# Kernel tuning notes

Measured on AMD Instinct MI355X. Metric: run time of the kernel, lower is better.

Reference implementation:

```python
import jax, jax.numpy as jnp
import numpy as np

# --- module constants (from init_kwargs) ---
R_HRS = 1000000.0   # high-resistance state (ohm)
R_LRS = 1000.0      # low-resistance state (ohm)
PARASITIC_R = 2.0   # wire resistance per crossbar segment (ohm)
BITS = 4            # conductance quantization bits
BATCH, IN_F, OUT_F = 8192, 1024, 1024


def weight_mapping(W, R_hrs, R_lrs):
    # linearly map weights into the [G_hrs, G_lrs] conductance window
    G_hrs, G_lrs = 1.0 / R_hrs, 1.0 / R_lrs
    Wmin, Wmax = W.min(), W.max()
    return (W - Wmin) / (Wmax - Wmin) * (G_lrs - G_hrs) + G_hrs


def quantization(G, R_lrs, R_hrs, bits):
    # snap conductances to 2**bits uniform levels in [G_hrs, G_lrs]
    G_hrs, G_lrs = 1.0 / R_hrs, 1.0 / R_lrs
    step = (G_lrs - G_hrs) / (2 ** bits - 1)
    return jnp.round((G - G_hrs) / step) * step + G_hrs


def ideal_model(G, x, parasitic_r):
    # ideal crossbar: I = V @ G  (no IR drop)
    return x @ G


def jeong_model(G, x, parasitic_r):
    # Jeong-style analytical IR-drop model: each cell (i, j) sees an extra
    # series wire resistance r*((j+1) segments along its word line +
    # (rows - i) segments along its bit line).
    rows, cols = G.shape  # [in, out]
    r_series = parasitic_r * (
        (jnp.arange(cols, dtype=G.dtype) + 1.0)[None, :]
        + (rows - jnp.arange(rows, dtype=G.dtype))[:, None]
    )  # [in, out]
    G_eff = 1.0 / (1.0 / G + r_series)
    return x @ G_eff  # [batch, out]


def output_unmapping(Wt, currents, x, R_hrs, R_lrs):
    # invert the affine conductance mapping: G = a*W + b  =>  x@W = (I - b*sum(x))/a
    G_hrs, G_lrs = 1.0 / R_hrs, 1.0 / R_lrs
    Wmin, Wmax = Wt.min(), Wt.max()
    a = (G_lrs - G_hrs) / (Wmax - Wmin)
    b = G_hrs - a * Wmin
    return (currents - b * x.sum(axis=1, keepdims=True)) / a


def setup_inputs() -> dict:
    key = jax.random.key(0)
    k1, k2, k3 = jax.random.split(key, 3)
    x = jax.random.uniform(k1, (BATCH, IN_F), dtype=jnp.float32)          # read voltages in [0,1)
    weight = jax.random.normal(k2, (OUT_F, IN_F), dtype=jnp.float32) * 0.1
    bias = jax.random.normal(k3, (OUT_F,), dtype=jnp.float32) * 0.01
    return {"x": x, "weight": weight, "bias": bias}


def reference(x, weight, bias):
    Wt = weight.T  # [in, out], matches self.weight.T in the torch module
    conductances = quantization(weight_mapping(Wt, R_HRS, R_LRS), R_LRS, R_HRS, BITS)
    currents = jeong_model(conductances, x, PARASITIC_R)          # non-ideal simulation
    ideal_currents = ideal_model(conductances, x, PARASITIC_R)    # bias-correction pass
    correction = currents.mean(axis=1) / ideal_currents.mean(axis=1)  # [batch]
    output = output_unmapping(Wt, currents, x, R_HRS, R_LRS)      # [batch, out]
    return output + bias[None, :] * correction[:, None]
```

## Files before the change

kernel.cpp:

```cpp
#include <hip/hip_runtime.h>
#include <hip/hip_bf16.h>
#include <cstdint>

#define BATCH 8192
#define IN_F  1024
#define OUT_F 1024
#define G_HRS 1e-6f
#define G_LRS 1e-3f
#define PAR_R 2.0f
#define LEVELS 15.0f

#define WS_MM    0
#define WS_VEFF  4096
#define WS_VID   8192
#define WS_CORR  16384
#define WS_BT    65536
#define WS_ABF   (65536 + 2097152)
#define WS_NEED_FULL  (WS_ABF + (size_t)BATCH * IN_F * 2)
#define WS_NEED_MIN   ((size_t)WS_ABF)

__device__ __forceinline__ unsigned short f2bf(float f) {
    union { float f; unsigned int i; } v; v.f = f;
    unsigned int u = v.i;
    unsigned int r = (u + 0x7FFFu + ((u >> 16) & 1u)) >> 16;
    return (unsigned short)r;
}
__device__ __forceinline__ unsigned int fmap(float f) {
    union { float f; unsigned int u; } v; v.f = f;
    return (v.u & 0x80000000u) ? ~v.u : (v.u | 0x80000000u);
}
__device__ __forceinline__ float funmap(unsigned int m) {
    union { unsigned int u; float f; } v;
    v.u = (m & 0x80000000u) ? (m & 0x7FFFFFFFu) : ~m;
    return v.f;
}
__device__ __forceinline__ float quant_g(float wv, float wmin, float inv_range) {
    float t = (wv - wmin) * inv_range;
    float step = (G_LRS - G_HRS) / LEVELS;
    return rintf(t * LEVELS) * step + G_HRS;
}

__global__ void kinit(unsigned int* mm) {
    if (threadIdx.x == 0) { mm[0] = 0u; mm[1] = 0xFFFFFFFFu; }
}

__global__ void kminmax(const float* __restrict__ w, unsigned int* mm) {
    int tid = blockIdx.x * blockDim.x + threadIdx.x;
    int stride = gridDim.x * blockDim.x;
    float lo = 1e30f, hi = -1e30f;
    const float4* w4 = (const float4*)w;
    const int n4 = (IN_F * OUT_F) / 4;
    for (int i = tid; i < n4; i += stride) {
        float4 q = w4[i];
        lo = fminf(lo, fminf(fminf(q.x, q.y), fminf(q.z, q.w)));
        hi = fmaxf(hi, fmaxf(fmaxf(q.x, q.y), fmaxf(q.z, q.w)));
    }
#pragma unroll
    for (int m = 1; m < 64; m <<= 1) {
        lo = fminf(lo, __shfl_xor(lo, m, 64));
        hi = fmaxf(hi, __shfl_xor(hi, m, 64));
    }
    if ((threadIdx.x & 63) == 0) {
        atomicMax(&mm[0], fmap(hi));
        atomicMin(&mm[1], fmap(lo));
    }
}

__global__ void kbuild(const float* __restrict__ w, const unsigned int* __restrict__ mm,
                       unsigned short* __restrict__ bt) {
    float wmax = funmap(mm[0]), wmin = funmap(mm[1]);
    float inv_range = 1.0f / (wmax - wmin);
    float acoef = (G_LRS - G_HRS) * inv_range;
    float bcoef = G_HRS - acoef * wmin;
    float inva = 1.0f / acoef;
    int n = blockIdx.x;
    int k0 = threadIdx.x * 4;
    float4 q = *(const float4*)&w[n * IN_F + k0];
    float wv[4] = { q.x, q.y, q.z, q.w };
    unsigned short o[4];
#pragma unroll
    for (int j = 0; j < 4; j++) {
        int k = k0 + j;
        float g = quant_g(wv[j], wmin, inv_range);
        float r = PAR_R * ((float)(n + 1) + (float)(IN_F - k));
        float ge = 1.0f / (1.0f / g + r);
        o[j] = f2bf((ge - bcoef) * inva);
    }
    uint2 ov;
    ov.x = (unsigned int)o[0] | ((unsigned int)o[1] << 16);
    ov.y = (unsigned int)o[2] | ((unsigned int)o[3] << 16);
    *(uint2*)&bt[n * IN_F + k0] = ov;
}

__global__ void kvec(const float* __restrict__ w, const unsigned int* __restrict__ mm,
                     float* __restrict__ veff, float* __restrict__ vid) {
    float wmax = funmap(mm[0]), wmin = funmap(mm[1]);
    float inv_range = 1.0f / (wmax - wmin);
    int k = blockIdx.x;
    float se = 0.f, si = 0.f;
    for (int n = threadIdx.x; n < OUT_F; n += blockDim.x) {
        float g = quant_g(w[n * IN_F + k], wmin, inv_range);
        float r = PAR_R * ((float)(n + 1) + (float)(IN_F - k));
        se += 1.0f / (1.0f / g + r);
        si += g;
    }
#pragma unroll
    for (int m = 1; m < 64; m <<= 1) {
        se += __shfl_xor(se, m, 64);
        si += __shfl_xor(si, m, 64);
    }
    __shared__ float red[8];
    int wv = threadIdx.x >> 6, ln = threadIdx.x & 63;
    if (ln == 0) { red[wv] = se; red[4 + wv] = si; }
    __syncthreads();
    if (threadIdx.x == 0) {
        veff[k] = red[0] + red[1] + red[2] + red[3];
        vid[k]  = red[4] + red[5] + red[6] + red[7];
    }
}

__global__ void kcorr(const float* __restrict__ x, const float* __restrict__ veff,
                      const float* __restrict__ vid, float* __restrict__ corr,
                      unsigned short* __restrict__ abf) {
    int row = blockIdx.x;
    int k0 = threadIdx.x * 4;
    float4 q = *(const float4*)&x[(size_t)row * IN_F + k0];
    if (abf) {
        uint2 ov;
        ov.x = (unsigned int)f2bf(q.x) | ((unsigned int)f2bf(q.y) << 16);
        ov.y = (unsigned int)f2bf(q.z) | ((unsigned int)f2bf(q.w) << 16);
        *(uint2*)&abf[(size_t)row * IN_F + k0] = ov;
    }
    float se = q.x * veff[k0] + q.y * veff[k0 + 1] + q.z * veff[k0 + 2] + q.w * veff[k0 + 3];
    float si = q.x * vid[k0]  + q.y * vid[k0 + 1]  + q.z * vid[k0 + 2]  + q.w * vid[k0 + 3];
#pragma unroll
    for (int m = 1; m < 64; m <<= 1) {
        se += __shfl_xor(se, m, 64);
        si += __shfl_xor(si, m, 64);
    }
    __shared__ float red[8];
    int wv = threadIdx.x >> 6, ln = threadIdx.x & 63;
    if (ln == 0) { red[wv] = se; red[4 + wv] = si; }
    __syncthreads();
    if (threadIdx.x == 0)
        corr[row] = (red[0] + red[1] + red[2] + red[3]) / (red[4] + red[5] + red[6] + red[7]);
}

typedef __attribute__((ext_vector_type(8))) short bf16x8;
typedef __attribute__((ext_vector_type(4))) float f32x4;

#define GLD_LDS16(g, l) \
    __builtin_amdgcn_global_load_lds((const __attribute__((address_space(1))) void*)(g), \
                                     (__attribute__((address_space(3))) void*)(l), 16, 0, 0)

template <bool CONVA>
__global__ __launch_bounds__(256) void kgemm(
    const float* __restrict__ Af32,
    const unsigned short* __restrict__ Abf,
    const unsigned short* __restrict__ Bt,
    const float* __restrict__ bias,
    const float* __restrict__ corr,
    float* __restrict__ out)
{
    __shared__ unsigned short As[128 * 32];
    __shared__ unsigned short Bs[128 * 32];
    const int tid = threadIdx.x;
    const int bm = blockIdx.x * 128;
    const int bn = blockIdx.y * 128;
    const int wave = tid >> 6, lane = tid & 63;
    const int wmL = (wave >> 1) * 64;
    const int wnL = (wave & 1) * 64;
    const int fr = lane & 15;
    const int fk = (lane >> 4) * 8;
    const int quad = lane >> 4;

    f32x4 acc[4][4] = {};

    const int c0 = tid, c1 = tid + 256;
    const unsigned short* gB0 = Bt + (size_t)(bn + (c0 >> 2)) * IN_F + ((c0 & 3) << 3);
    const unsigned short* gB1 = Bt + (size_t)(bn + (c1 >> 2)) * IN_F + ((c1 & 3) << 3);
    const unsigned short* gA0 = nullptr; const unsigned short* gA1 = nullptr;
    const float* fA0 = nullptr; const float* fA1 = nullptr;
    if (CONVA) {
        fA0 = Af32 + (size_t)(bm + (c0 >> 2)) * IN_F + ((c0 & 3) << 3);
        fA1 = Af32 + (size_t)(bm + (c1 >> 2)) * IN_F + ((c1 & 3) << 3);
    } else {
        gA0 = Abf + (size_t)(bm + (c0 >> 2)) * IN_F + ((c0 & 3) << 3);
        gA1 = Abf + (size_t)(bm + (c1 >> 2)) * IN_F + ((c1 & 3) << 3);
    }

    for (int kb = 0; kb < IN_F; kb += 32) {
        uint2 cv0, cv1;
        if (CONVA) {
            float4 p0 = *(const float4*)(fA0 + kb);
            float4 p1 = *(const float4*)(fA0 + kb + 4);
            float4 p2 = *(const float4*)(fA1 + kb);
            float4 p3 = *(const float4*)(fA1 + kb + 4);
            cv0.x = (unsigned int)f2bf(p0.x) | ((unsigned int)f2bf(p0.y) << 16);
            cv0.y = (unsigned int)f2bf(p0.z) | ((unsigned int)f2bf(p0.w) << 16);
            uint2 cv0b; cv0b.x = (unsigned int)f2bf(p1.x) | ((unsigned int)f2bf(p1.y) << 16);
            cv0b.y = (unsigned int)f2bf(p1.z) | ((unsigned int)f2bf(p1.w) << 16);
            uint2 cv1a; cv1a.x = (unsigned int)f2bf(p2.x) | ((unsigned int)f2bf(p2.y) << 16);
            cv1a.y = (unsigned int)f2bf(p2.z) | ((unsigned int)f2bf(p2.w) << 16);
            uint2 cv1b; cv1b.x = (unsigned int)f2bf(p3.x) | ((unsigned int)f2bf(p3.y) << 16);
            cv1b.y = (unsigned int)f2bf(p3.z) | ((unsigned int)f2bf(p3.w) << 16);
            __syncthreads();
            *(uint4*)&As[c0 * 8] = make_uint4(cv0.x, cv0.y, cv0b.x, cv0b.y);
            *(uint4*)&As[c1 * 8] = make_uint4(cv1a.x, cv1a.y, cv1b.x, cv1b.y);
            GLD_LDS16(gB0 + kb, &Bs[c0 * 8]);
            GLD_LDS16(gB1 + kb, &Bs[c1 * 8]);
        } else {
            __syncthreads();
            GLD_LDS16(gA0 + kb, &As[c0 * 8]);
            GLD_LDS16(gA1 + kb, &As[c1 * 8]);
            GLD_LDS16(gB0 + kb, &Bs[c0 * 8]);
            GLD_LDS16(gB1 + kb, &Bs[c1 * 8]);
        }
        __syncthreads();

        bf16x8 af[4], bfv[4];
#pragma unroll
        for (int mt = 0; mt < 4; mt++)
            af[mt] = *(const bf16x8*)&As[(wmL + mt * 16 + fr) * 32 + fk];
#pragma unroll
        for (int nt = 0; nt < 4; nt++)
            bfv[nt] = *(const bf16x8*)&Bs[(wnL + nt * 16 + fr) * 32 + fk];
#pragma unroll
        for (int mt = 0; mt < 4; mt++)
#pragma unroll
            for (int nt = 0; nt < 4; nt++)
                acc[mt][nt] = __builtin_amdgcn_mfma_f32_16x16x32_bf16(af[mt], bfv[nt], acc[mt][nt], 0, 0, 0);
    }

#pragma unroll
    for (int nt = 0; nt < 4; nt++) {
        int gc = bn + wnL + nt * 16 + fr;
        float bv = bias[gc];
#pragma unroll
        for (int mt = 0; mt < 4; mt++) {
#pragma unroll
            for (int r = 0; r < 4; r++) {
                int gr = bm + wmL + mt * 16 + quad * 4 + r;
                out[(size_t)gr * OUT_F + gc] = acc[mt][nt][r] + bv * corr[gr];
            }
        }
    }
}

extern "C" void kernel_launch(void* const* d_in, const int* in_sizes, int n_in,
                              void* d_out, int out_size, void* d_ws, size_t ws_size,
                              hipStream_t stream) {
    const float* x    = (const float*)d_in[0];
    const float* w    = (const float*)d_in[1];
    const float* bias = (const float*)d_in[2];
    float* out = (float*)d_out;

    char* ws = (char*)d_ws;
    unsigned int* mm   = (unsigned int*)(ws + WS_MM);
    float* veff        = (float*)(ws + WS_VEFF);
    float* vid         = (float*)(ws + WS_VID);
    float* corr        = (float*)(ws + WS_CORR);
    unsigned short* bt = (unsigned short*)(ws + WS_BT);
    unsigned short* abf = (unsigned short*)(ws + WS_ABF);

    bool full = ws_size >= WS_NEED_FULL;

    kinit<<<1, 64, 0, stream>>>(mm);
    kminmax<<<256, 256, 0, stream>>>(w, mm);
    kbuild<<<OUT_F, 256, 0, stream>>>(w, mm, bt);
    kvec<<<IN_F, 256, 0, stream>>>(w, mm, veff, vid);
    kcorr<<<BATCH, 256, 0, stream>>>(x, veff, vid, corr, full ? abf : nullptr);
    if (full)
        kgemm<false><<<dim3(BATCH / 128, OUT_F / 128), 256, 0, stream>>>(x, abf, bt, bias, corr, out);
    else
        kgemm<true><<<dim3(BATCH / 128, OUT_F / 128), 256, 0, stream>>>(x, nullptr, bt, bias, corr, out);
}
```

Before: 154.5 us.

## Fuse weight preprocessing kernels and swap GEMM grid order

Merges the min/max reduction, init, B-matrix build and column-sum kernels into two kernels. Per-block partial min/max replaces the global atomics, and the column sums are accumulated with atomicAdd inside the build kernel, which removes the strided column-walk kernel (kvec). The GEMM grid now puts the output-column dimension in blockIdx.x, so consecutive blocks share A rows for better L2 reuse. The float atomic sums make veff/vid ordering nondeterministic, and the change cuts launch count and redundant reads of the weights.

```diff
diff --git a/kernel.cpp b/kernel.cpp
--- a/kernel.cpp
+++ b/kernel.cpp
@@ -10,14 +10,14 @@
 #define PAR_R 2.0f
 #define LEVELS 15.0f
 
-#define WS_MM    0
+#define WS_PMIN  0
+#define WS_PMAX  1024
 #define WS_VEFF  4096
 #define WS_VID   8192
 #define WS_CORR  16384
 #define WS_BT    65536
 #define WS_ABF   (65536 + 2097152)
-#define WS_NEED_FULL  (WS_ABF + (size_t)BATCH * IN_F * 2)
-#define WS_NEED_MIN   ((size_t)WS_ABF)
+#define WS_NEED_FULL  ((size_t)WS_ABF + (size_t)BATCH * IN_F * 2)
 
 __device__ __forceinline__ unsigned short f2bf(float f) {
     union { float f; unsigned int i; } v; v.f = f;
@@ -25,32 +25,19 @@
     unsigned int r = (u + 0x7FFFu + ((u >> 16) & 1u)) >> 16;
     return (unsigned short)r;
 }
-__device__ __forceinline__ unsigned int fmap(float f) {
-    union { float f; unsigned int u; } v; v.f = f;
-    return (v.u & 0x80000000u) ? ~v.u : (v.u | 0x80000000u);
-}
-__device__ __forceinline__ float funmap(unsigned int m) {
-    union { unsigned int u; float f; } v;
-    v.u = (m & 0x80000000u) ? (m & 0x7FFFFFFFu) : ~m;
-    return v.f;
-}
 __device__ __forceinline__ float quant_g(float wv, float wmin, float inv_range) {
     float t = (wv - wmin) * inv_range;
     float step = (G_LRS - G_HRS) / LEVELS;
     return rintf(t * LEVELS) * step + G_HRS;
 }
 
-__global__ void kinit(unsigned int* mm) {
-    if (threadIdx.x == 0) { mm[0] = 0u; mm[1] = 0xFFFFFFFFu; }
-}
-
-__global__ void kminmax(const float* __restrict__ w, unsigned int* mm) {
+__global__ void kprep(const float* __restrict__ w, float* __restrict__ pmin, float* __restrict__ pmax,
+                      float* __restrict__ veff, float* __restrict__ vid) {
     int tid = blockIdx.x * blockDim.x + threadIdx.x;
-    int stride = gridDim.x * blockDim.x;
     float lo = 1e30f, hi = -1e30f;
     const float4* w4 = (const float4*)w;
     const int n4 = (IN_F * OUT_F) / 4;
-    for (int i = tid; i < n4; i += stride) {
+    for (int i = tid; i < n4; i += 256 * 256) {
         float4 q = w4[i];
         lo = fminf(lo, fminf(fminf(q.x, q.y), fminf(q.z, q.w)));
         hi = fmaxf(hi, fmaxf(fmaxf(q.x, q.y), fmaxf(q.z, q.w)));
@@ -60,62 +47,69 @@
         lo = fminf(lo, __shfl_xor(lo, m, 64));
         hi = fmaxf(hi, __shfl_xor(hi, m, 64));
     }
-    if ((threadIdx.x & 63) == 0) {
-        atomicMax(&mm[0], fmap(hi));
-        atomicMin(&mm[1], fmap(lo));
-    }
-}
-
-__global__ void kbuild(const float* __restrict__ w, const unsigned int* __restrict__ mm,
-                       unsigned short* __restrict__ bt) {
-    float wmax = funmap(mm[0]), wmin = funmap(mm[1]);
+    __shared__ float slo[4], shi[4];
+    int wv = threadIdx.x >> 6, ln = threadIdx.x & 63;
+    if (ln == 0) { slo[wv] = lo; shi[wv] = hi; }
+    __syncthreads();
+    if (threadIdx.x == 0) {
+        pmin[blockIdx.x] = fminf(fminf(slo[0], slo[1]), fminf(slo[2], slo[3]));
+        pmax[blockIdx.x] = fmaxf(fmaxf(shi[0], shi[1]), fmaxf(shi[2], shi[3]));
+    }
+    if (blockIdx.x == 0) {
+        float4 z = make_float4(0.f, 0.f, 0.f, 0.f);
+        ((float4*)veff)[threadIdx.x] = z;
+        ((float4*)vid)[threadIdx.x]  = z;
+    }
+}
+
+__global__ void kbuildvec(const float* __restrict__ w, const float* __restrict__ pmin,
+                          const float* __restrict__ pmax, unsigned short* __restrict__ bt,
+                          float* __restrict__ veff, float* __restrict__ vid) {
+    float lo = pmin[threadIdx.x], hi = pmax[threadIdx.x];
+#pragma unroll
+    for (int m = 1; m < 64; m <<= 1) {
+        lo = fminf(lo, __shfl_xor(lo, m, 64));
+        hi = fmaxf(hi, __shfl_xor(hi, m, 64));
+    }
+    __shared__ float slo[4], shi[4];
+    int wv = threadIdx.x >> 6, ln = threadIdx.x & 63;
+    if (ln == 0) { slo[wv] = lo; shi[wv] = hi; }
+    __syncthreads();
+    float wmin = fminf(fminf(slo[0], slo[1]), fminf(slo[2], slo[3]));
+    float wmax = fmaxf(fmaxf(shi[0], shi[1]), fmaxf(shi[2], shi[3]));
+
     float inv_range = 1.0f / (wmax - wmin);
     float acoef = (G_LRS - G_HRS) * inv_range;
     float bcoef = G_HRS - acoef * wmin;
     float inva = 1.0f / acoef;
-    int n = blockIdx.x;
+
     int k0 = threadIdx.x * 4;
-    float4 q = *(const float4*)&w[n * IN_F + k0];
-    float wv[4] = { q.x, q.y, q.z, q.w };
-    unsigned short o[4];
+    float se[4] = {0.f, 0.f, 0.f, 0.f}, si[4] = {0.f, 0.f, 0.f, 0.f};
+#pragma unroll
+    for (int rr = 0; rr < 4; rr++) {
+        int n = blockIdx.x * 4 + rr;
+        float4 q = *(const float4*)&w[(size_t)n * IN_F + k0];
+        float wvv[4] = { q.x, q.y, q.z, q.w };
+        unsigned short o[4];
+#pragma unroll
+        for (int j = 0; j < 4; j++) {
+            int k = k0 + j;
+            float g = quant_g(wvv[j], wmin, inv_range);
+            float r = PAR_R * ((float)(n + 1) + (float)(IN_F - k));
+            float ge = 1.0f / (1.0f / g + r);
+            o[j] = f2bf((ge - bcoef) * inva);
+            se[j] += ge;
+            si[j] += g;
+        }
+        uint2 ov;
+        ov.x = (unsigned int)o[0] | ((unsigned int)o[1] << 16);
+        ov.y = (unsigned int)o[2] | ((unsigned int)o[3] << 16);
+        *(uint2*)&bt[(size_t)n * IN_F + k0] = ov;
+    }
 #pragma unroll
     for (int j = 0; j < 4; j++) {
-        int k = k0 + j;
-        float g = quant_g(wv[j], wmin, inv_range);
-        float r = PAR_R * ((float)(n + 1) + (float)(IN_F - k));
-        float ge = 1.0f / (1.0f / g + r);
-        o[j] = f2bf((ge - bcoef) * inva);
-    }
-    uint2 ov;
-    ov.x = (unsigned int)o[0] | ((unsigned int)o[1] << 16);
-    ov.y = (unsigned int)o[2] | ((unsigned int)o[3] << 16);
-    *(uint2*)&bt[n * IN_F + k0] = ov;
-}
-
-__global__ void kvec(const float* __restrict__ w, const unsigned int* __restrict__ mm,
-                     float* __restrict__ veff, float* __restrict__ vid) {
-    float wmax = funmap(mm[0]), wmin = funmap(mm[1]);
-    float inv_range = 1.0f / (wmax - wmin);
-    int k = blockIdx.x;
-    float se = 0.f, si = 0.f;
-    for (int n = threadIdx.x; n < OUT_F; n += blockDim.x) {
-        float g = quant_g(w[n * IN_F + k], wmin, inv_range);
-        float r = PAR_R * ((float)(n + 1) + (float)(IN_F - k));
-        se += 1.0f / (1.0f / g + r);
-        si += g;
-    }
-#pragma unroll
-    for (int m = 1; m < 64; m <<= 1) {
-        se += __shfl_xor(se, m, 64);
-        si += __shfl_xor(si, m, 64);
-    }
-    __shared__ float red[8];
-    int wv = threadIdx.x >> 6, ln = threadIdx.x & 63;
-    if (ln == 0) { red[wv] = se; red[4 + wv] = si; }
-    __syncthreads();
-    if (threadIdx.x == 0) {
-        veff[k] = red[0] + red[1] + red[2] + red[3];
-        vid[k]  = red[4] + red[5] + red[6] + red[7];
+        atomicAdd(&veff[k0 + j], se[j]);
+        atomicAdd(&vid[k0 + j], si[j]);
     }
 }
 
@@ -131,8 +125,10 @@
         ov.y = (unsigned int)f2bf(q.z) | ((unsigned int)f2bf(q.w) << 16);
         *(uint2*)&abf[(size_t)row * IN_F + k0] = ov;
     }
-    float se = q.x * veff[k0] + q.y * veff[k0 + 1] + q.z * veff[k0 + 2] + q.w * veff[k0 + 3];
-    float si = q.x * vid[k0]  + q.y * vid[k0 + 1]  + q.z * vid[k0 + 2]  + q.w * vid[k0 + 3];
+    float4 ve = *(const float4*)&veff[k0];
+    float4 vi = *(const float4*)&vid[k0];
+    float se = q.x * ve.x + q.y * ve.y + q.z * ve.z + q.w * ve.w;
+    float si = q.x * vi.x + q.y * vi.y + q.z * vi.z + q.w * vi.w;
 #pragma unroll
     for (int m = 1; m < 64; m <<= 1) {
         se += __shfl_xor(se, m, 64);
@@ -165,8 +161,8 @@
     __shared__ unsigned short As[128 * 32];
     __shared__ unsigned short Bs[128 * 32];
     const int tid = threadIdx.x;
-    const int bm = blockIdx.x * 128;
-    const int bn = blockIdx.y * 128;
+    const int bn = blockIdx.x * 128;
+    const int bm = blockIdx.y * 128;
     const int wave = tid >> 6, lane = tid & 63;
     const int wmL = (wave >> 1) * 64;
     const int wnL = (wave & 1) * 64;
@@ -190,23 +186,24 @@
     }
 
     for (int kb = 0; kb < IN_F; kb += 32) {
-        uint2 cv0, cv1;
         if (CONVA) {
             float4 p0 = *(const float4*)(fA0 + kb);
             float4 p1 = *(const float4*)(fA0 + kb + 4);
             float4 p2 = *(const float4*)(fA1 + kb);
             float4 p3 = *(const float4*)(fA1 + kb + 4);
-            cv0.x = (unsigned int)f2bf(p0.x) | ((unsigned int)f2bf(p0.y) << 16);
-            cv0.y = (unsigned int)f2bf(p0.z) | ((unsigned int)f2bf(p0.w) << 16);
-            uint2 cv0b; cv0b.x = (unsigned int)f2bf(p1.x) | ((unsigned int)f2bf(p1.y) << 16);
-            cv0b.y = (unsigned int)f2bf(p1.z) | ((unsigned int)f2bf(p1.w) << 16);
-            uint2 cv1a; cv1a.x = (unsigned int)f2bf(p2.x) | ((unsigned int)f2bf(p2.y) << 16);
-            cv1a.y = (unsigned int)f2bf(p2.z) | ((unsigned int)f2bf(p2.w) << 16);
-            uint2 cv1b; cv1b.x = (unsigned int)f2bf(p3.x) | ((unsigned int)f2bf(p3.y) << 16);
-            cv1b.y = (unsigned int)f2bf(p3.z) | ((unsigned int)f2bf(p3.w) << 16);
+            uint4 u0 = make_uint4(
+                (unsigned int)f2bf(p0.x) | ((unsigned int)f2bf(p0.y) << 16),
+                (unsigned int)f2bf(p0.z) | ((unsigned int)f2bf(p0.w) << 16),
+                (unsigned int)f2bf(p1.x) | ((unsigned int)f2bf(p1.y) << 16),
+                (unsigned int)f2bf(p1.z) | ((unsigned int)f2bf(p1.w) << 16));
+            uint4 u1 = make_uint4(
+                (unsigned int)f2bf(p2.x) | ((unsigned int)f2bf(p2.y) << 16),
+                (unsigned int)f2bf(p2.z) | ((unsigned int)f2bf(p2.w) << 16),
+                (unsigned int)f2bf(p3.x) | ((unsigned int)f2bf(p3.y) << 16),
+                (unsigned int)f2bf(p3.z) | ((unsigned int)f2bf(p3.w) << 16));
             __syncthreads();
-            *(uint4*)&As[c0 * 8] = make_uint4(cv0.x, cv0.y, cv0b.x, cv0b.y);
-            *(uint4*)&As[c1 * 8] = make_uint4(cv1a.x, cv1a.y, cv1b.x, cv1b.y);
+            *(uint4*)&As[c0 * 8] = u0;
+            *(uint4*)&As[c1 * 8] = u1;
             GLD_LDS16(gB0 + kb, &Bs[c0 * 8]);
             GLD_LDS16(gB1 + kb, &Bs[c1 * 8]);
         } else {
@@ -256,7 +253,8 @@
     float* out = (float*)d_out;
 
     char* ws = (char*)d_ws;
-    unsigned int* mm   = (unsigned int*)(ws + WS_MM);
+    float* pmin        = (float*)(ws + WS_PMIN);
+    float* pmax        = (float*)(ws + WS_PMAX);
     float* veff        = (float*)(ws + WS_VEFF);
     float* vid         = (float*)(ws + WS_VID);
     float* corr        = (float*)(ws + WS_CORR);
@@ -265,13 +263,11 @@
 
     bool full = ws_size >= WS_NEED_FULL;
 
-    kinit<<<1, 64, 0, stream>>>(mm);
-    kminmax<<<256, 256, 0, stream>>>(w, mm);
-    kbuild<<<OUT_F, 256, 0, stream>>>(w, mm, bt);
-    kvec<<<IN_F, 256, 0, stream>>>(w, mm, veff, vid);
+    kprep<<<256, 256, 0, stream>>>(w, pmin, pmax, veff, vid);
+    kbuildvec<<<OUT_F / 4, 256, 0, stream>>>(w, pmin, pmax, bt, veff, vid);
     kcorr<<<BATCH, 256, 0, stream>>>(x, veff, vid, corr, full ? abf : nullptr);
     if (full)
-        kgemm<false><<<dim3(BATCH / 128, OUT_F / 128), 256, 0, stream>>>(x, abf, bt, bias, corr, out);
+        kgemm<false><<<dim3(OUT_F / 128, BATCH / 128), 256, 0, stream>>>(x, abf, bt, bias, corr, out);
     else
-        kgemm<true><<<dim3(BATCH / 128, OUT_F / 128), 256, 0, stream>>>(x, nullptr, bt, bias, corr, out);
-}
+        kgemm<true><<<dim3(OUT_F / 128, BATCH / 128), 256, 0, stream>>>(x, nullptr, bt, bias, corr, out);
+}
```

After: 148.1 us. 1.04x faster.
